# Kernel optimization log

Measured on AMD Instinct MI355X. Metric: run time of the kernel, lower is better.

Reference implementation:

```python
import jax, jax.numpy as jnp
import numpy as np

ALPHA = 1.702
EPS_RMS = 1e-6
W_LOAD = 0.01
W_IMP = 0.01
W_AUX = 1.0
LIMIT = 7.0
K_TOP = 4


def swiglu(x, alpha=ALPHA, limit=LIMIT):
    x_glu = jnp.clip(x[..., ::2], -limit, limit)
    x_lin = jnp.clip(x[..., 1::2], -limit, limit)
    return x_glu * jax.nn.sigmoid(x_glu * alpha) + (x_lin + 1.0)


def setup_inputs() -> dict:
    key = jax.random.key(0)
    ks = jax.random.split(key, 4)
    T, H, I, E = 2048, 512, 512, 8
    x = jax.random.normal(ks[0], (T, H), dtype=jnp.float32)
    norm_scale = jnp.ones((H,), jnp.float32)
    gate_w = jax.random.normal(ks[1], (E, H), jnp.float32) * 0.02
    gate_b = jnp.zeros((E,), jnp.float32)
    mlp1_w = jax.random.normal(ks[2], (E, 2 * I, H), jnp.float32) * 0.02
    mlp1_b = jnp.zeros((E, 2 * I), jnp.float32)
    mlp2_w = jax.random.normal(ks[3], (E, H, I), jnp.float32) * 0.02
    mlp2_b = jnp.zeros((E, H), jnp.float32)
    return {"x": x, "norm_scale": norm_scale, "gate_w": gate_w, "gate_b": gate_b,
            "mlp1_w": mlp1_w, "mlp1_b": mlp1_b, "mlp2_w": mlp2_w, "mlp2_b": mlp2_b}


def reference(x, norm_scale, gate_w, gate_b, mlp1_w, mlp1_b, mlp2_w, mlp2_b):
    T, H = x.shape
    E = gate_w.shape[0]
    K = K_TOP
    # RMSNorm (fp32 math as in torch module)
    t = x * jax.lax.rsqrt(jnp.mean(x * x, axis=-1, keepdims=True) + EPS_RMS) * norm_scale
    # gating
    gate_logits = t @ gate_w.T + gate_b                      # [T, E]
    gate_probs = jax.nn.softmax(gate_logits, axis=-1)
    expert_weights, experts_indices = jax.lax.top_k(gate_probs, K)
    expert_weights = expert_weights / expert_weights.sum(axis=-1, keepdims=True)
    # per-token per-expert combine coefficient (sum of slot weights routed to e)
    coeff = jnp.zeros((T, E), x.dtype).at[jnp.arange(T)[:, None], experts_indices].add(expert_weights)
    # dense expert compute (math-equivalent to the gathered einsums; avoids
    # materializing per-token weight matrices)
    h = jnp.einsum('th,ech->tec', t, mlp1_w) + mlp1_b[None]  # [T, E, 2I]
    a = swiglu(h)                                            # [T, E, I]
    y = jnp.einsum('tei,ehi->teh', a, mlp2_w) + mlp2_b[None] # [T, E, H]
    out = jnp.einsum('teh,te->th', y, coeff) + x
    # aux losses (replicates the torch code exactly, incl. D-doubling quirk)
    P = gate_probs.mean(axis=0)                              # [E]
    counts = jax.vmap(lambda col: jnp.zeros((E,), x.dtype).at[col].add(1.0), in_axes=1)(experts_indices)  # [K, E]
    doubling = (2.0 ** (K - jnp.arange(K))).astype(x.dtype)  # D_i = 2*(D_{i-1}+c_i)
    D = (doubling[:, None] * counts).sum(axis=0) / (T * K)
    loss_load = W_LOAD * E * (P * D).sum()
    importance = gate_logits.sum(axis=0)
    cv = jnp.std(importance, ddof=1) / (importance.mean() + 1e-6)
    loss_imp = W_IMP * cv ** 2
    aux_loss = W_AUX * (loss_load + loss_imp)
    return out, aux_loss
```

## Files before the change

kernel.cpp:

```cpp
#include <hip/hip_runtime.h>
#include <stdint.h>

#define ALPHA 1.702f
#define LIMIT 7.0f

typedef float f32x4 __attribute__((ext_vector_type(4)));
typedef __bf16 bf16x8 __attribute__((ext_vector_type(8)));

static __device__ __forceinline__ unsigned short f2bf(float f) {
    union { float f; uint32_t u; } v; v.f = f;
    uint32_t u = v.u;
    return (unsigned short)((u + 0x7FFFu + ((u >> 16) & 1u)) >> 16);
}

#define GLL16(GP, LP) __builtin_amdgcn_global_load_lds( \
    (const __attribute__((address_space(1))) void*)(GP), \
    (__attribute__((address_space(3))) void*)(LP), 16, 0, 0)

static __device__ __forceinline__ int lsw(int row, int kc) {
    return row * 4 + (kc ^ ((row >> 1) & 3));
}

__global__ __launch_bounds__(256) void prep_kernel(
    const float* __restrict__ w1, const float* __restrict__ w2,
    unsigned short* __restrict__ w1p, unsigned short* __restrict__ w2b,
    const float* __restrict__ x,
    const float* __restrict__ norm_scale,
    const float* __restrict__ gate_w,
    const float* __restrict__ gate_b,
    const float* __restrict__ b2,
    unsigned short* __restrict__ t_bf,
    float* __restrict__ coeff,
    float* __restrict__ accum,
    float* __restrict__ out)
{
    __shared__ float red[4][48];
    if (blockIdx.x < 6144) {
        const int idx = blockIdx.x * 256 + threadIdx.x;
        const int n1 = 1048576;
        if (idx < n1) {
            const int e = idx >> 17;
            const int rem = idx & 131071;
            const int r = rem >> 7;
            const int c = rem & 127;
            const int src = (r < 512) ? (2 * r) : (2 * (r - 512) + 1);
            float4 v = ((const float4*)w1)[(e << 17) + (src << 7) + c];
            ushort4 o = { f2bf(v.x), f2bf(v.y), f2bf(v.z), f2bf(v.w) };
            ((ushort4*)w1p)[idx] = o;
        } else {
            const int i2 = idx - n1;
            float4 v = ((const float4*)w2)[i2];
            ushort4 o = { f2bf(v.x), f2bf(v.y), f2bf(v.z), f2bf(v.w) };
            ((ushort4*)w2b)[i2] = o;
        }
        return;
    }
    const int bid = blockIdx.x - 6144;
    const int wave = threadIdx.x >> 6;
    const int lane = threadIdx.x & 63;

    float accP[8], accI[8], accC[32];
    #pragma unroll
    for (int e = 0; e < 8; ++e) { accP[e] = 0.f; accI[e] = 0.f; }
    #pragma unroll
    for (int i = 0; i < 32; ++i) accC[i] = 0.f;

    #pragma unroll
    for (int it = 0; it < 2; ++it) {
        const int t = bid * 8 + wave * 2 + it;
        const float4* xr = (const float4*)(x + t * 512);
        float4 x0 = xr[lane * 2];
        float4 x1 = xr[lane * 2 + 1];
        float ss = x0.x*x0.x + x0.y*x0.y + x0.z*x0.z + x0.w*x0.w
                 + x1.x*x1.x + x1.y*x1.y + x1.z*x1.z + x1.w*x1.w;
        #pragma unroll
        for (int off = 32; off > 0; off >>= 1) ss += __shfl_xor(ss, off, 64);
        const float rstd = rsqrtf(ss * (1.f / 512.f) + 1e-6f);
        const float4* sr = (const float4*)norm_scale;
        float4 s0 = sr[lane * 2], s1 = sr[lane * 2 + 1];
        float tv[8];
        tv[0] = x0.x * rstd * s0.x; tv[1] = x0.y * rstd * s0.y;
        tv[2] = x0.z * rstd * s0.z; tv[3] = x0.w * rstd * s0.w;
        tv[4] = x1.x * rstd * s1.x; tv[5] = x1.y * rstd * s1.y;
        tv[6] = x1.z * rstd * s1.z; tv[7] = x1.w * rstd * s1.w;
        uint32_t p0 = (uint32_t)f2bf(tv[0]) | ((uint32_t)f2bf(tv[1]) << 16);
        uint32_t p1 = (uint32_t)f2bf(tv[2]) | ((uint32_t)f2bf(tv[3]) << 16);
        uint32_t p2 = (uint32_t)f2bf(tv[4]) | ((uint32_t)f2bf(tv[5]) << 16);
        uint32_t p3 = (uint32_t)f2bf(tv[6]) | ((uint32_t)f2bf(tv[7]) << 16);
        uint4 pk; pk.x = p0; pk.y = p1; pk.z = p2; pk.w = p3;
        ((uint4*)(t_bf + t * 512))[lane] = pk;
        float le[8];
        #pragma unroll
        for (int e = 0; e < 8; ++e) {
            const float4* gw = (const float4*)(gate_w + e * 512);
            float4 g0 = gw[lane * 2], g1 = gw[lane * 2 + 1];
            float d = tv[0]*g0.x + tv[1]*g0.y + tv[2]*g0.z + tv[3]*g0.w
                    + tv[4]*g1.x + tv[5]*g1.y + tv[6]*g1.z + tv[7]*g1.w;
            #pragma unroll
            for (int off = 32; off > 0; off >>= 1) d += __shfl_xor(d, off, 64);
            le[e] = d + gate_b[e];
        }
        float mx = le[0];
        #pragma unroll
        for (int e = 1; e < 8; ++e) mx = fmaxf(mx, le[e]);
        float pe[8], se = 0.f;
        #pragma unroll
        for (int e = 0; e < 8; ++e) { pe[e] = __expf(le[e] - mx); se += pe[e]; }
        const float sinv = 1.f / se;
        #pragma unroll
        for (int e = 0; e < 8; ++e) pe[e] *= sinv;
        unsigned picked = 0;
        int ik[4]; float wk[4];
        #pragma unroll
        for (int k = 0; k < 4; ++k) {
            float bv = -1.f; int bi = 0;
            #pragma unroll
            for (int e = 0; e < 8; ++e)
                if (!(picked & (1u << e)) && pe[e] > bv) { bv = pe[e]; bi = e; }
            ik[k] = bi; wk[k] = bv; picked |= (1u << bi);
        }
        const float winv = 1.f / (wk[0] + wk[1] + wk[2] + wk[3]);
        float nw[4];
        #pragma unroll
        for (int k = 0; k < 4; ++k) nw[k] = wk[k] * winv;
        float ce[8];
        #pragma unroll
        for (int e = 0; e < 8; ++e) {
            float c = 0.f;
            #pragma unroll
            for (int k = 0; k < 4; ++k) c += (ik[k] == e) ? nw[k] : 0.f;
            ce[e] = c;
        }
        if (lane == 0) {
            #pragma unroll
            for (int e = 0; e < 8; ++e) coeff[t * 8 + e] = ce[e];
        }
        #pragma unroll
        for (int e = 0; e < 8; ++e) { accP[e] += pe[e]; accI[e] += le[e]; }
        #pragma unroll
        for (int k = 0; k < 4; ++k)
            #pragma unroll
            for (int e = 0; e < 8; ++e)
                accC[k * 8 + e] += (ik[k] == e) ? 1.f : 0.f;
        float ov[8];
        ov[0] = x0.x; ov[1] = x0.y; ov[2] = x0.z; ov[3] = x0.w;
        ov[4] = x1.x; ov[5] = x1.y; ov[6] = x1.z; ov[7] = x1.w;
        #pragma unroll
        for (int e = 0; e < 8; ++e) {
            const float4* br = (const float4*)(b2 + e * 512);
            float4 b0 = br[lane * 2], bb1 = br[lane * 2 + 1];
            ov[0] += ce[e] * b0.x; ov[1] += ce[e] * b0.y;
            ov[2] += ce[e] * b0.z; ov[3] += ce[e] * b0.w;
            ov[4] += ce[e] * bb1.x; ov[5] += ce[e] * bb1.y;
            ov[6] += ce[e] * bb1.z; ov[7] += ce[e] * bb1.w;
        }
        float4 o0, o1;
        o0.x = ov[0]; o0.y = ov[1]; o0.z = ov[2]; o0.w = ov[3];
        o1.x = ov[4]; o1.y = ov[5]; o1.z = ov[6]; o1.w = ov[7];
        float4* orow = (float4*)(out + t * 512);
        orow[lane * 2] = o0; orow[lane * 2 + 1] = o1;
    }
    if (lane == 0) {
        #pragma unroll
        for (int e = 0; e < 8; ++e) { red[wave][e] = accP[e]; red[wave][8 + e] = accI[e]; }
        #pragma unroll
        for (int i = 0; i < 32; ++i) red[wave][16 + i] = accC[i];
    }
    __syncthreads();
    if (threadIdx.x < 48) {
        float s = red[0][threadIdx.x] + red[1][threadIdx.x]
                + red[2][threadIdx.x] + red[3][threadIdx.x];
        atomicAdd(accum + threadIdx.x, s);
    }
}

__global__ __launch_bounds__(256, 2) void gemm1_swiglu(
    const unsigned short* __restrict__ A,
    const unsigned short* __restrict__ w1p,
    const float* __restrict__ b1,
    const float* __restrict__ coeff,
    unsigned short* __restrict__ As,
    const float* __restrict__ accum,
    float* __restrict__ aux_out)
{
    if (blockIdx.x == 512) {
        if (threadIdx.x == 0) {
            float imp[8], sl = 0.f;
            #pragma unroll
            for (int e = 0; e < 8; ++e) {
                float P = accum[e] * (1.f / 2048.f);
                imp[e] = accum[8 + e];
                float D = (16.f * accum[16 + e] + 8.f * accum[24 + e]
                         + 4.f * accum[32 + e] + 2.f * accum[40 + e]) * (1.f / 8192.f);
                sl += P * D;
            }
            float loss_load = 0.01f * 8.f * sl;
            float mean = 0.f;
            #pragma unroll
            for (int e = 0; e < 8; ++e) mean += imp[e];
            mean *= 0.125f;
            float var = 0.f;
            #pragma unroll
            for (int e = 0; e < 8; ++e) { float d = imp[e] - mean; var += d * d; }
            var *= (1.f / 7.f);
            float cv = sqrtf(var) / (mean + 1e-6f);
            *aux_out = loss_load + 0.01f * cv * cv;
        }
        return;
    }
    __shared__ unsigned short tA[2][4096];
    __shared__ unsigned short tBg[2][4096];
    __shared__ unsigned short tBl[2][4096];
    const int tid = threadIdx.x;
    const int bx = blockIdx.x;
    const int tile_p = bx & 31, tile_m = bx >> 5;
    const int e = tile_p >> 2;
    const int np = (tile_p & 3) * 128;
    const int m0 = tile_m * 128;
    const int lane = tid & 63, wave = tid >> 6;
    const int wm = (wave & 1) * 64, wn = (wave >> 1) * 64;
    const int quad = lane >> 4, l16 = lane & 15;
    const int srow = tid >> 2;
    const int soff = ((tid & 3) ^ ((tid >> 3) & 3)) * 8;

    const unsigned short* Ar0 = A + (m0 + srow) * 512 + soff;
    const unsigned short* Ar1 = A + (m0 + 64 + srow) * 512 + soff;
    const unsigned short* Bg = w1p + (e * 1024 + np) * 512;
    const unsigned short* Bg0 = Bg + srow * 512 + soff;
    const unsigned short* Bg1 = Bg + (64 + srow) * 512 + soff;
    const unsigned short* Bl0 = Bg0 + 512 * 512;
    const unsigned short* Bl1 = Bg1 + 512 * 512;

    int rA[4], rB[4];
    #pragma unroll
    for (int i = 0; i < 4; ++i) {
        rA[i] = lsw(wm + i * 16 + l16, quad) * 8;
        rB[i] = lsw(wn + i * 16 + l16, quad) * 8;
    }

    f32x4 accG[4][4], accL[4][4];
    #pragma unroll
    for (int i = 0; i < 4; ++i)
        #pragma unroll
        for (int j = 0; j < 4; ++j) {
            f32x4 z = {0.f, 0.f, 0.f, 0.f};
            accG[i][j] = z; accL[i][j] = z;
        }

#define STAGE1(s, k0) do { \
    GLL16(Ar0 + (k0), tA[s] + tid * 8); \
    GLL16(Ar1 + (k0), tA[s] + (tid + 256) * 8); \
    GLL16(Bg0 + (k0), tBg[s] + tid * 8); \
    GLL16(Bg1 + (k0), tBg[s] + (tid + 256) * 8); \
    GLL16(Bl0 + (k0), tBl[s] + tid * 8); \
    GLL16(Bl1 + (k0), tBl[s] + (tid + 256) * 8); \
} while (0)

    STAGE1(0, 0);
    STAGE1(1, 32);
    #pragma unroll
    for (int kt = 0; kt < 16; ++kt) {
        const int cur = kt & 1;
        if (kt < 15) asm volatile("s_waitcnt vmcnt(6)" ::: "memory");
        else         asm volatile("s_waitcnt vmcnt(0)" ::: "memory");
        asm volatile("s_barrier" ::: "memory");
        bf16x8 af[4], bg[4], bl[4];
        #pragma unroll
        for (int i = 0; i < 4; ++i) {
            af[i] = *(const bf16x8*)(tA[cur] + rA[i]);
            bg[i] = *(const bf16x8*)(tBg[cur] + rB[i]);
            bl[i] = *(const bf16x8*)(tBl[cur] + rB[i]);
        }
        asm volatile("s_waitcnt lgkmcnt(0)" ::: "memory");
        asm volatile("s_barrier" ::: "memory");
        if (kt < 14) STAGE1(cur, (kt + 2) * 32);
        #pragma unroll
        for (int i = 0; i < 4; ++i)
            #pragma unroll
            for (int j = 0; j < 4; ++j) {
                accG[i][j] = __builtin_amdgcn_mfma_f32_16x16x32_bf16(af[i], bg[j], accG[i][j], 0, 0, 0);
                accL[i][j] = __builtin_amdgcn_mfma_f32_16x16x32_bf16(af[i], bl[j], accL[i][j], 0, 0, 0);
            }
    }
#undef STAGE1

    float cw[4][4];
    #pragma unroll
    for (int i = 0; i < 4; ++i) {
        const int rowb = m0 + wm + i * 16 + quad * 4;
        #pragma unroll
        for (int r = 0; r < 4; ++r) cw[i][r] = coeff[(rowb + r) * 8 + e];
    }
    #pragma unroll
    for (int j = 0; j < 4; ++j) {
        const int colp = np + wn + j * 16 + l16;
        const float bgv = b1[e * 1024 + 2 * colp];
        const float blv = b1[e * 1024 + 2 * colp + 1];
        #pragma unroll
        for (int i = 0; i < 4; ++i) {
            const int rowb = m0 + wm + i * 16 + quad * 4;
            #pragma unroll
            for (int r = 0; r < 4; ++r) {
                float g = fminf(fmaxf(accG[i][j][r] + bgv, -LIMIT), LIMIT);
                float l = fminf(fmaxf(accL[i][j][r] + blv, -LIMIT), LIMIT);
                float a = g / (1.f + __expf(-ALPHA * g)) + l + 1.f;
                a *= cw[i][r];
                As[(rowb + r) * 4096 + e * 512 + colp] = f2bf(a);
            }
        }
    }
}

__global__ __launch_bounds__(256, 2) void gemm2(
    const unsigned short* __restrict__ As,
    const unsigned short* __restrict__ w2b,
    float* __restrict__ out)
{
    __shared__ unsigned short tA[2][4096];
    __shared__ unsigned short tB[2][4096];
    const int tid = threadIdx.x;
    const int bx = blockIdx.x;
    const int tile_n = bx & 3;
    const int tile_m = (bx >> 2) & 15;
    const int e = bx >> 6;
    const int m0 = tile_m * 128, n0 = tile_n * 128;
    const int lane = tid & 63, wave = tid >> 6;
    const int wm = (wave & 1) * 64, wn = (wave >> 1) * 64;
    const int quad = lane >> 4, l16 = lane & 15;
    const int srow = tid >> 2;
    const int soff = ((tid & 3) ^ ((tid >> 3) & 3)) * 8;

    const unsigned short* Ar0 = As + (m0 + srow) * 4096 + e * 512 + soff;
    const unsigned short* Ar1 = As + (m0 + 64 + srow) * 4096 + e * 512 + soff;
    const unsigned short* Bb  = w2b + e * 262144;
    const unsigned short* Br0 = Bb + (n0 + srow) * 512 + soff;
    const unsigned short* Br1 = Bb + (n0 + 64 + srow) * 512 + soff;

    int rA[4], rB[4];
    #pragma unroll
    for (int i = 0; i < 4; ++i) {
        rA[i] = lsw(wm + i * 16 + l16, quad) * 8;
        rB[i] = lsw(wn + i * 16 + l16, quad) * 8;
    }

    f32x4 acc[4][4];
    #pragma unroll
    for (int i = 0; i < 4; ++i)
        #pragma unroll
        for (int j = 0; j < 4; ++j) { f32x4 z = {0.f, 0.f, 0.f, 0.f}; acc[i][j] = z; }

#define STAGE2(s, k0) do { \
    GLL16(Ar0 + (k0), tA[s] + tid * 8); \
    GLL16(Ar1 + (k0), tA[s] + (tid + 256) * 8); \
    GLL16(Br0 + (k0), tB[s] + tid * 8); \
    GLL16(Br1 + (k0), tB[s] + (tid + 256) * 8); \
} while (0)

    STAGE2(0, 0);
    STAGE2(1, 32);
    #pragma unroll
    for (int kt = 0; kt < 16; ++kt) {
        const int cur = kt & 1;
        if (kt < 15) asm volatile("s_waitcnt vmcnt(4)" ::: "memory");
        else         asm volatile("s_waitcnt vmcnt(0)" ::: "memory");
        asm volatile("s_barrier" ::: "memory");
        bf16x8 af[4], bf[4];
        #pragma unroll
        for (int i = 0; i < 4; ++i) {
            af[i] = *(const bf16x8*)(tA[cur] + rA[i]);
            bf[i] = *(const bf16x8*)(tB[cur] + rB[i]);
        }
        asm volatile("s_waitcnt lgkmcnt(0)" ::: "memory");
        asm volatile("s_barrier" ::: "memory");
        if (kt < 14) STAGE2(cur, (kt + 2) * 32);
        #pragma unroll
        for (int i = 0; i < 4; ++i)
            #pragma unroll
            for (int j = 0; j < 4; ++j)
                acc[i][j] = __builtin_amdgcn_mfma_f32_16x16x32_bf16(af[i], bf[j], acc[i][j], 0, 0, 0);
    }
#undef STAGE2

    #pragma unroll
    for (int j = 0; j < 4; ++j) {
        const int col = n0 + wn + j * 16 + l16;
        #pragma unroll
        for (int i = 0; i < 4; ++i) {
            const int rowb = m0 + wm + i * 16 + quad * 4;
            #pragma unroll
            for (int r = 0; r < 4; ++r)
                atomicAdd(&out[(rowb + r) * 512 + col], acc[i][j][r]);
        }
    }
}

extern "C" void kernel_launch(void* const* d_in, const int* in_sizes, int n_in,
                              void* d_out, int out_size, void* d_ws, size_t ws_size,
                              hipStream_t stream)
{
    (void)in_sizes; (void)n_in; (void)out_size; (void)ws_size;
    const float* x          = (const float*)d_in[0];
    const float* norm_scale = (const float*)d_in[1];
    const float* gate_w     = (const float*)d_in[2];
    const float* gate_b     = (const float*)d_in[3];
    const float* mlp1_w     = (const float*)d_in[4];
    const float* mlp1_b     = (const float*)d_in[5];
    const float* mlp2_w     = (const float*)d_in[6];
    const float* mlp2_b     = (const float*)d_in[7];
    float* out = (float*)d_out;

    char* ws = (char*)d_ws;
    unsigned short* w1p   = (unsigned short*)(ws);
    unsigned short* w2b   = (unsigned short*)(ws + 8388608);
    unsigned short* tbf   = (unsigned short*)(ws + 12582912);
    unsigned short* As    = (unsigned short*)(ws + 14680064);
    float*          coeff = (float*)(ws + 31457280);
    float*          accum = (float*)(ws + 31522816);

    hipMemsetAsync(accum, 0, 192, stream);
    prep_kernel<<<6400, 256, 0, stream>>>(mlp1_w, mlp2_w, w1p, w2b,
                                          x, norm_scale, gate_w, gate_b, mlp2_b,
                                          tbf, coeff, accum, out);
    gemm1_swiglu<<<513, 256, 0, stream>>>(tbf, w1p, mlp1_b, coeff, As,
                                          accum, out + 2048 * 512);
    gemm2<<<512, 256, 0, stream>>>(As, w2b, out);
}
```

Measured before the change: 166.8 us.

## Fuse gemm1 and gemm2 into one persistent kernel with per-tile dependency flags

```diff
diff --git a/kernel.cpp b/kernel.cpp
--- a/kernel.cpp
+++ b/kernel.cpp
@@ -31,11 +31,13 @@
     const float* __restrict__ b2,
     unsigned short* __restrict__ t_bf,
     float* __restrict__ coeff,
-    float* __restrict__ accum,
+    float* __restrict__ paux,
+    int* __restrict__ done,
     float* __restrict__ out)
 {
     __shared__ float red[4][48];
     if (blockIdx.x < 6144) {
+        if (blockIdx.x == 0 && threadIdx.x < 128) done[threadIdx.x & 127] = 0;
         const int idx = blockIdx.x * 256 + threadIdx.x;
         const int n1 = 1048576;
         if (idx < n1) {
@@ -168,69 +170,33 @@
     }
     __syncthreads();
     if (threadIdx.x < 48) {
-        float s = red[0][threadIdx.x] + red[1][threadIdx.x]
-                + red[2][threadIdx.x] + red[3][threadIdx.x];
-        atomicAdd(accum + threadIdx.x, s);
+        paux[bid * 48 + threadIdx.x] =
+            red[0][threadIdx.x] + red[1][threadIdx.x]
+          + red[2][threadIdx.x] + red[3][threadIdx.x];
     }
 }
 
-__global__ __launch_bounds__(256, 2) void gemm1_swiglu(
+__global__ __launch_bounds__(256, 2) void fused_gemm(
     const unsigned short* __restrict__ A,
     const unsigned short* __restrict__ w1p,
     const float* __restrict__ b1,
     const float* __restrict__ coeff,
     unsigned short* __restrict__ As,
-    const float* __restrict__ accum,
-    float* __restrict__ aux_out)
+    const unsigned short* __restrict__ w2b,
+    float* __restrict__ out,
+    const float* __restrict__ paux,
+    float* __restrict__ aux_out,
+    int* __restrict__ done)
 {
-    if (blockIdx.x == 512) {
-        if (threadIdx.x == 0) {
-            float imp[8], sl = 0.f;
-            #pragma unroll
-            for (int e = 0; e < 8; ++e) {
-                float P = accum[e] * (1.f / 2048.f);
-                imp[e] = accum[8 + e];
-                float D = (16.f * accum[16 + e] + 8.f * accum[24 + e]
-                         + 4.f * accum[32 + e] + 2.f * accum[40 + e]) * (1.f / 8192.f);
-                sl += P * D;
-            }
-            float loss_load = 0.01f * 8.f * sl;
-            float mean = 0.f;
-            #pragma unroll
-            for (int e = 0; e < 8; ++e) mean += imp[e];
-            mean *= 0.125f;
-            float var = 0.f;
-            #pragma unroll
-            for (int e = 0; e < 8; ++e) { float d = imp[e] - mean; var += d * d; }
-            var *= (1.f / 7.f);
-            float cv = sqrtf(var) / (mean + 1e-6f);
-            *aux_out = loss_load + 0.01f * cv * cv;
-        }
-        return;
-    }
-    __shared__ unsigned short tA[2][4096];
-    __shared__ unsigned short tBg[2][4096];
-    __shared__ unsigned short tBl[2][4096];
+    __shared__ unsigned short smem[6][4608];
     const int tid = threadIdx.x;
     const int bx = blockIdx.x;
-    const int tile_p = bx & 31, tile_m = bx >> 5;
-    const int e = tile_p >> 2;
-    const int np = (tile_p & 3) * 128;
-    const int m0 = tile_m * 128;
     const int lane = tid & 63, wave = tid >> 6;
     const int wm = (wave & 1) * 64, wn = (wave >> 1) * 64;
     const int quad = lane >> 4, l16 = lane & 15;
     const int srow = tid >> 2;
     const int soff = ((tid & 3) ^ ((tid >> 3) & 3)) * 8;
 
-    const unsigned short* Ar0 = A + (m0 + srow) * 512 + soff;
-    const unsigned short* Ar1 = A + (m0 + 64 + srow) * 512 + soff;
-    const unsigned short* Bg = w1p + (e * 1024 + np) * 512;
-    const unsigned short* Bg0 = Bg + srow * 512 + soff;
-    const unsigned short* Bg1 = Bg + (64 + srow) * 512 + soff;
-    const unsigned short* Bl0 = Bg0 + 512 * 512;
-    const unsigned short* Bl1 = Bg1 + 512 * 512;
-
     int rA[4], rB[4];
     #pragma unroll
     for (int i = 0; i < 4; ++i) {
@@ -238,158 +204,197 @@
         rB[i] = lsw(wn + i * 16 + l16, quad) * 8;
     }
 
-    f32x4 accG[4][4], accL[4][4];
-    #pragma unroll
-    for (int i = 0; i < 4; ++i)
-        #pragma unroll
-        for (int j = 0; j < 4; ++j) {
-            f32x4 z = {0.f, 0.f, 0.f, 0.f};
-            accG[i][j] = z; accL[i][j] = z;
-        }
+    {
+        const int tile_p = bx & 31, tile_m = bx >> 5;
+        const int e = tile_p >> 2;
+        const int np = (tile_p & 3) * 128;
+        const int m0 = tile_m * 128;
+
+        const unsigned short* Ar0 = A + (m0 + srow) * 512 + soff;
+        const unsigned short* Ar1 = A + (m0 + 64 + srow) * 512 + soff;
+        const unsigned short* Bg = w1p + (e * 1024 + np) * 512;
+        const unsigned short* Bg0 = Bg + srow * 512 + soff;
+        const unsigned short* Bg1 = Bg + (64 + srow) * 512 + soff;
+        const unsigned short* Bl0 = Bg0 + 512 * 512;
+        const unsigned short* Bl1 = Bg1 + 512 * 512;
+
+        f32x4 accG[4][4], accL[4][4];
+        #pragma unroll
+        for (int i = 0; i < 4; ++i)
+            #pragma unroll
+            for (int j = 0; j < 4; ++j) {
+                f32x4 z = {0.f, 0.f, 0.f, 0.f};
+                accG[i][j] = z; accL[i][j] = z;
+            }
 
 #define STAGE1(s, k0) do { \
-    GLL16(Ar0 + (k0), tA[s] + tid * 8); \
-    GLL16(Ar1 + (k0), tA[s] + (tid + 256) * 8); \
-    GLL16(Bg0 + (k0), tBg[s] + tid * 8); \
-    GLL16(Bg1 + (k0), tBg[s] + (tid + 256) * 8); \
-    GLL16(Bl0 + (k0), tBl[s] + tid * 8); \
-    GLL16(Bl1 + (k0), tBl[s] + (tid + 256) * 8); \
+    GLL16(Ar0 + (k0), smem[(s)*3+0] + tid * 8); \
+    GLL16(Ar1 + (k0), smem[(s)*3+0] + (tid + 256) * 8); \
+    GLL16(Bg0 + (k0), smem[(s)*3+1] + tid * 8); \
+    GLL16(Bg1 + (k0), smem[(s)*3+1] + (tid + 256) * 8); \
+    GLL16(Bl0 + (k0), smem[(s)*3+2] + tid * 8); \
+    GLL16(Bl1 + (k0), smem[(s)*3+2] + (tid + 256) * 8); \
 } while (0)
 
-    STAGE1(0, 0);
-    STAGE1(1, 32);
-    #pragma unroll
-    for (int kt = 0; kt < 16; ++kt) {
-        const int cur = kt & 1;
-        if (kt < 15) asm volatile("s_waitcnt vmcnt(6)" ::: "memory");
-        else         asm volatile("s_waitcnt vmcnt(0)" ::: "memory");
-        asm volatile("s_barrier" ::: "memory");
-        bf16x8 af[4], bg[4], bl[4];
-        #pragma unroll
-        for (int i = 0; i < 4; ++i) {
-            af[i] = *(const bf16x8*)(tA[cur] + rA[i]);
-            bg[i] = *(const bf16x8*)(tBg[cur] + rB[i]);
-            bl[i] = *(const bf16x8*)(tBl[cur] + rB[i]);
-        }
-        asm volatile("s_waitcnt lgkmcnt(0)" ::: "memory");
-        asm volatile("s_barrier" ::: "memory");
-        if (kt < 14) STAGE1(cur, (kt + 2) * 32);
-        #pragma unroll
-        for (int i = 0; i < 4; ++i)
-            #pragma unroll
-            for (int j = 0; j < 4; ++j) {
-                accG[i][j] = __builtin_amdgcn_mfma_f32_16x16x32_bf16(af[i], bg[j], accG[i][j], 0, 0, 0);
-                accL[i][j] = __builtin_amdgcn_mfma_f32_16x16x32_bf16(af[i], bl[j], accL[i][j], 0, 0, 0);
-            }
-    }
+        STAGE1(0, 0);
+        STAGE1(1, 32);
+        #pragma unroll
+        for (int kt = 0; kt < 16; ++kt) {
+            const int cur = kt & 1;
+            if (kt < 15) asm volatile("s_waitcnt vmcnt(6)" ::: "memory");
+            else         asm volatile("s_waitcnt vmcnt(0)" ::: "memory");
+            asm volatile("s_barrier" ::: "memory");
+            bf16x8 af[4], bg[4], bl[4];
+            #pragma unroll
+            for (int i = 0; i < 4; ++i) {
+                af[i] = *(const bf16x8*)(smem[cur*3+0] + rA[i]);
+                bg[i] = *(const bf16x8*)(smem[cur*3+1] + rB[i]);
+                bl[i] = *(const bf16x8*)(smem[cur*3+2] + rB[i]);
+            }
+            asm volatile("s_waitcnt lgkmcnt(0)" ::: "memory");
+            asm volatile("s_barrier" ::: "memory");
+            if (kt < 14) STAGE1(cur, (kt + 2) * 32);
+            #pragma unroll
+            for (int i = 0; i < 4; ++i)
+                #pragma unroll
+                for (int j = 0; j < 4; ++j) {
+                    accG[i][j] = __builtin_amdgcn_mfma_f32_16x16x32_bf16(af[i], bg[j], accG[i][j], 0, 0, 0);
+                    accL[i][j] = __builtin_amdgcn_mfma_f32_16x16x32_bf16(af[i], bl[j], accL[i][j], 0, 0, 0);
+                }
+        }
 #undef STAGE1
 
-    float cw[4][4];
-    #pragma unroll
-    for (int i = 0; i < 4; ++i) {
-        const int rowb = m0 + wm + i * 16 + quad * 4;
-        #pragma unroll
-        for (int r = 0; r < 4; ++r) cw[i][r] = coeff[(rowb + r) * 8 + e];
-    }
-    #pragma unroll
-    for (int j = 0; j < 4; ++j) {
-        const int colp = np + wn + j * 16 + l16;
-        const float bgv = b1[e * 1024 + 2 * colp];
-        const float blv = b1[e * 1024 + 2 * colp + 1];
+        float cw[4][4];
         #pragma unroll
         for (int i = 0; i < 4; ++i) {
             const int rowb = m0 + wm + i * 16 + quad * 4;
             #pragma unroll
-            for (int r = 0; r < 4; ++r) {
-                float g = fminf(fmaxf(accG[i][j][r] + bgv, -LIMIT), LIMIT);
-                float l = fminf(fmaxf(accL[i][j][r] + blv, -LIMIT), LIMIT);
-                float a = g / (1.f + __expf(-ALPHA * g)) + l + 1.f;
-                a *= cw[i][r];
-                As[(rowb + r) * 4096 + e * 512 + colp] = f2bf(a);
-            }
-        }
-    }
-}
-
-__global__ __launch_bounds__(256, 2) void gemm2(
-    const unsigned short* __restrict__ As,
-    const unsigned short* __restrict__ w2b,
-    float* __restrict__ out)
-{
-    __shared__ unsigned short tA[2][4096];
-    __shared__ unsigned short tB[2][4096];
-    const int tid = threadIdx.x;
-    const int bx = blockIdx.x;
-    const int tile_n = bx & 3;
-    const int tile_m = (bx >> 2) & 15;
-    const int e = bx >> 6;
-    const int m0 = tile_m * 128, n0 = tile_n * 128;
-    const int lane = tid & 63, wave = tid >> 6;
-    const int wm = (wave & 1) * 64, wn = (wave >> 1) * 64;
-    const int quad = lane >> 4, l16 = lane & 15;
-    const int srow = tid >> 2;
-    const int soff = ((tid & 3) ^ ((tid >> 3) & 3)) * 8;
-
-    const unsigned short* Ar0 = As + (m0 + srow) * 4096 + e * 512 + soff;
-    const unsigned short* Ar1 = As + (m0 + 64 + srow) * 4096 + e * 512 + soff;
-    const unsigned short* Bb  = w2b + e * 262144;
-    const unsigned short* Br0 = Bb + (n0 + srow) * 512 + soff;
-    const unsigned short* Br1 = Bb + (n0 + 64 + srow) * 512 + soff;
-
-    int rA[4], rB[4];
-    #pragma unroll
-    for (int i = 0; i < 4; ++i) {
-        rA[i] = lsw(wm + i * 16 + l16, quad) * 8;
-        rB[i] = lsw(wn + i * 16 + l16, quad) * 8;
-    }
-
-    f32x4 acc[4][4];
-    #pragma unroll
-    for (int i = 0; i < 4; ++i)
-        #pragma unroll
-        for (int j = 0; j < 4; ++j) { f32x4 z = {0.f, 0.f, 0.f, 0.f}; acc[i][j] = z; }
+            for (int r = 0; r < 4; ++r) cw[i][r] = coeff[(rowb + r) * 8 + e];
+        }
+        #pragma unroll
+        for (int j = 0; j < 4; ++j) {
+            const int colp = np + wn + j * 16 + l16;
+            const float bgv = b1[e * 1024 + 2 * colp];
+            const float blv = b1[e * 1024 + 2 * colp + 1];
+            #pragma unroll
+            for (int i = 0; i < 4; ++i) {
+                const int rowb = m0 + wm + i * 16 + quad * 4;
+                #pragma unroll
+                for (int r = 0; r < 4; ++r) {
+                    float g = fminf(fmaxf(accG[i][j][r] + bgv, -LIMIT), LIMIT);
+                    float l = fminf(fmaxf(accL[i][j][r] + blv, -LIMIT), LIMIT);
+                    float a = g / (1.f + __expf(-ALPHA * g)) + l + 1.f;
+                    a *= cw[i][r];
+                    As[(rowb + r) * 4096 + e * 512 + colp] = f2bf(a);
+                }
+            }
+        }
+        __threadfence();
+        __syncthreads();
+        if (tid == 0)
+            __hip_atomic_fetch_add(&done[tile_m * 8 + e], 1,
+                                   __ATOMIC_RELEASE, __HIP_MEMORY_SCOPE_AGENT);
+    }
+
+    if (bx == 0) {
+        float* sred = (float*)(smem[5] + 4096);
+        if (tid < 48) {
+            float s = 0.f;
+            for (int b = 0; b < 256; ++b) s += paux[b * 48 + tid];
+            sred[tid] = s;
+        }
+        __syncthreads();
+        if (tid == 0) {
+            float imp[8], sl = 0.f;
+            #pragma unroll
+            for (int e = 0; e < 8; ++e) {
+                float P = sred[e] * (1.f / 2048.f);
+                imp[e] = sred[8 + e];
+                float D = (16.f * sred[16 + e] + 8.f * sred[24 + e]
+                         + 4.f * sred[32 + e] + 2.f * sred[40 + e]) * (1.f / 8192.f);
+                sl += P * D;
+            }
+            float loss_load = 0.01f * 8.f * sl;
+            float mean = 0.f;
+            #pragma unroll
+            for (int e = 0; e < 8; ++e) mean += imp[e];
+            mean *= 0.125f;
+            float var = 0.f;
+            #pragma unroll
+            for (int e = 0; e < 8; ++e) { float d = imp[e] - mean; var += d * d; }
+            var *= (1.f / 7.f);
+            float cv = sqrtf(var) / (mean + 1e-6f);
+            *aux_out = loss_load + 0.01f * cv * cv;
+        }
+    }
+
+    {
+        const int tile_n = bx & 3;
+        const int tile_m = (bx >> 2) & 15;
+        const int e = bx >> 6;
+        const int m0 = tile_m * 128, n0 = tile_n * 128;
+
+        if (tid == 0) {
+            while (__hip_atomic_load(&done[tile_m * 8 + e],
+                                     __ATOMIC_ACQUIRE, __HIP_MEMORY_SCOPE_AGENT) < 4)
+                __builtin_amdgcn_s_sleep(2);
+        }
+        __syncthreads();
+
+        const unsigned short* Ar0 = As + (m0 + srow) * 4096 + e * 512 + soff;
+        const unsigned short* Ar1 = As + (m0 + 64 + srow) * 4096 + e * 512 + soff;
+        const unsigned short* Bb  = w2b + e * 262144;
+        const unsigned short* Br0 = Bb + (n0 + srow) * 512 + soff;
+        const unsigned short* Br1 = Bb + (n0 + 64 + srow) * 512 + soff;
+
+        f32x4 acc[4][4];
+        #pragma unroll
+        for (int i = 0; i < 4; ++i)
+            #pragma unroll
+            for (int j = 0; j < 4; ++j) { f32x4 z = {0.f, 0.f, 0.f, 0.f}; acc[i][j] = z; }
 
 #define STAGE2(s, k0) do { \
-    GLL16(Ar0 + (k0), tA[s] + tid * 8); \
-    GLL16(Ar1 + (k0), tA[s] + (tid + 256) * 8); \
-    GLL16(Br0 + (k0), tB[s] + tid * 8); \
-    GLL16(Br1 + (k0), tB[s] + (tid + 256) * 8); \
+    GLL16(Ar0 + (k0), smem[(s)*3+0] + tid * 8); \
+    GLL16(Ar1 + (k0), smem[(s)*3+0] + (tid + 256) * 8); \
+    GLL16(Br0 + (k0), smem[(s)*3+1] + tid * 8); \
+    GLL16(Br1 + (k0), smem[(s)*3+1] + (tid + 256) * 8); \
 } while (0)
 
-    STAGE2(0, 0);
-    STAGE2(1, 32);
-    #pragma unroll
-    for (int kt = 0; kt < 16; ++kt) {
-        const int cur = kt & 1;
-        if (kt < 15) asm volatile("s_waitcnt vmcnt(4)" ::: "memory");
-        else         asm volatile("s_waitcnt vmcnt(0)" ::: "memory");
-        asm volatile("s_barrier" ::: "memory");
-        bf16x8 af[4], bf[4];
-        #pragma unroll
-        for (int i = 0; i < 4; ++i) {
-            af[i] = *(const bf16x8*)(tA[cur] + rA[i]);
-            bf[i] = *(const bf16x8*)(tB[cur] + rB[i]);
-        }
-        asm volatile("s_waitcnt lgkmcnt(0)" ::: "memory");
-        asm volatile("s_barrier" ::: "memory");
-        if (kt < 14) STAGE2(cur, (kt + 2) * 32);
-        #pragma unroll
-        for (int i = 0; i < 4; ++i)
-            #pragma unroll
-            for (int j = 0; j < 4; ++j)
-                acc[i][j] = __builtin_amdgcn_mfma_f32_16x16x32_bf16(af[i], bf[j], acc[i][j], 0, 0, 0);
-    }
+        STAGE2(0, 0);
+        STAGE2(1, 32);
+        #pragma unroll
+        for (int kt = 0; kt < 16; ++kt) {
+            const int cur = kt & 1;
+            if (kt < 15) asm volatile("s_waitcnt vmcnt(4)" ::: "memory");
+            else         asm volatile("s_waitcnt vmcnt(0)" ::: "memory");
+            asm volatile("s_barrier" ::: "memory");
+            bf16x8 af[4], bf[4];
+            #pragma unroll
+            for (int i = 0; i < 4; ++i) {
+                af[i] = *(const bf16x8*)(smem[cur*3+0] + rA[i]);
+                bf[i] = *(const bf16x8*)(smem[cur*3+1] + rB[i]);
+            }
+            asm volatile("s_waitcnt lgkmcnt(0)" ::: "memory");
+            asm volatile("s_barrier" ::: "memory");
+            if (kt < 14) STAGE2(cur, (kt + 2) * 32);
+            #pragma unroll
+            for (int i = 0; i < 4; ++i)
+                #pragma unroll
+                for (int j = 0; j < 4; ++j)
+                    acc[i][j] = __builtin_amdgcn_mfma_f32_16x16x32_bf16(af[i], bf[j], acc[i][j], 0, 0, 0);
+        }
 #undef STAGE2
 
-    #pragma unroll
-    for (int j = 0; j < 4; ++j) {
-        const int col = n0 + wn + j * 16 + l16;
-        #pragma unroll
-        for (int i = 0; i < 4; ++i) {
-            const int rowb = m0 + wm + i * 16 + quad * 4;
-            #pragma unroll
-            for (int r = 0; r < 4; ++r)
-                atomicAdd(&out[(rowb + r) * 512 + col], acc[i][j][r]);
+        #pragma unroll
+        for (int j = 0; j < 4; ++j) {
+            const int col = n0 + wn + j * 16 + l16;
+            #pragma unroll
+            for (int i = 0; i < 4; ++i) {
+                const int rowb = m0 + wm + i * 16 + quad * 4;
+                #pragma unroll
+                for (int r = 0; r < 4; ++r)
+                    atomicAdd(&out[(rowb + r) * 512 + col], acc[i][j][r]);
+            }
         }
     }
 }
@@ -415,13 +420,12 @@
     unsigned short* tbf   = (unsigned short*)(ws + 12582912);
     unsigned short* As    = (unsigned short*)(ws + 14680064);
     float*          coeff = (float*)(ws + 31457280);
-    float*          accum = (float*)(ws + 31522816);
-
-    hipMemsetAsync(accum, 0, 192, stream);
+    float*          paux  = (float*)(ws + 31522816);
+    int*            done  = (int*)(ws + 31571968);
+
     prep_kernel<<<6400, 256, 0, stream>>>(mlp1_w, mlp2_w, w1p, w2b,
                                           x, norm_scale, gate_w, gate_b, mlp2_b,
-                                          tbf, coeff, accum, out);
-    gemm1_swiglu<<<513, 256, 0, stream>>>(tbf, w1p, mlp1_b, coeff, As,
-                                          accum, out + 2048 * 512);
-    gemm2<<<512, 256, 0, stream>>>(As, w2b, out);
+                                          tbf, coeff, paux, done, out);
+    fused_gemm<<<512, 256, 0, stream>>>(tbf, w1p, mlp1_b, coeff, As, w2b, out,
+                                        paux, out + 2048 * 512, done);
 }
```

After: 251.4 us. 1.51x slower.

## Enlarge gemm1 tiles, deepen gemm2 pipeline, replace aux atomics with partials

Applied to the files above, without the earlier changes.

```diff
diff --git a/kernel.cpp b/kernel.cpp
--- a/kernel.cpp
+++ b/kernel.cpp
@@ -31,7 +31,7 @@
     const float* __restrict__ b2,
     unsigned short* __restrict__ t_bf,
     float* __restrict__ coeff,
-    float* __restrict__ accum,
+    float* __restrict__ paux,
     float* __restrict__ out)
 {
     __shared__ float red[4][48];
@@ -168,81 +168,55 @@
     }
     __syncthreads();
     if (threadIdx.x < 48) {
-        float s = red[0][threadIdx.x] + red[1][threadIdx.x]
-                + red[2][threadIdx.x] + red[3][threadIdx.x];
-        atomicAdd(accum + threadIdx.x, s);
-    }
-}
-
-__global__ __launch_bounds__(256, 2) void gemm1_swiglu(
+        paux[bid * 48 + threadIdx.x] =
+            red[0][threadIdx.x] + red[1][threadIdx.x]
+          + red[2][threadIdx.x] + red[3][threadIdx.x];
+    }
+}
+
+__global__ __launch_bounds__(256, 1) void gemm1_swiglu(
     const unsigned short* __restrict__ A,
     const unsigned short* __restrict__ w1p,
     const float* __restrict__ b1,
     const float* __restrict__ coeff,
-    unsigned short* __restrict__ As,
-    const float* __restrict__ accum,
-    float* __restrict__ aux_out)
+    unsigned short* __restrict__ As)
 {
-    if (blockIdx.x == 512) {
-        if (threadIdx.x == 0) {
-            float imp[8], sl = 0.f;
-            #pragma unroll
-            for (int e = 0; e < 8; ++e) {
-                float P = accum[e] * (1.f / 2048.f);
-                imp[e] = accum[8 + e];
-                float D = (16.f * accum[16 + e] + 8.f * accum[24 + e]
-                         + 4.f * accum[32 + e] + 2.f * accum[40 + e]) * (1.f / 8192.f);
-                sl += P * D;
-            }
-            float loss_load = 0.01f * 8.f * sl;
-            float mean = 0.f;
-            #pragma unroll
-            for (int e = 0; e < 8; ++e) mean += imp[e];
-            mean *= 0.125f;
-            float var = 0.f;
-            #pragma unroll
-            for (int e = 0; e < 8; ++e) { float d = imp[e] - mean; var += d * d; }
-            var *= (1.f / 7.f);
-            float cv = sqrtf(var) / (mean + 1e-6f);
-            *aux_out = loss_load + 0.01f * cv * cv;
-        }
-        return;
-    }
-    __shared__ unsigned short tA[2][4096];
+    __shared__ unsigned short tA[2][8192];
     __shared__ unsigned short tBg[2][4096];
     __shared__ unsigned short tBl[2][4096];
     const int tid = threadIdx.x;
     const int bx = blockIdx.x;
-    const int tile_p = bx & 31, tile_m = bx >> 5;
-    const int e = tile_p >> 2;
-    const int np = (tile_p & 3) * 128;
-    const int m0 = tile_m * 128;
+    const int g = bx & 31;
+    const int e = g >> 2;
+    const int np = (g & 3) * 128;
+    const int m0 = (bx >> 5) * 256;
     const int lane = tid & 63, wave = tid >> 6;
-    const int wm = (wave & 1) * 64, wn = (wave >> 1) * 64;
+    const int wm = wave * 64;
     const int quad = lane >> 4, l16 = lane & 15;
     const int srow = tid >> 2;
     const int soff = ((tid & 3) ^ ((tid >> 3) & 3)) * 8;
 
     const unsigned short* Ar0 = A + (m0 + srow) * 512 + soff;
     const unsigned short* Ar1 = A + (m0 + 64 + srow) * 512 + soff;
+    const unsigned short* Ar2 = A + (m0 + 128 + srow) * 512 + soff;
+    const unsigned short* Ar3 = A + (m0 + 192 + srow) * 512 + soff;
     const unsigned short* Bg = w1p + (e * 1024 + np) * 512;
     const unsigned short* Bg0 = Bg + srow * 512 + soff;
     const unsigned short* Bg1 = Bg + (64 + srow) * 512 + soff;
     const unsigned short* Bl0 = Bg0 + 512 * 512;
     const unsigned short* Bl1 = Bg1 + 512 * 512;
 
-    int rA[4], rB[4];
-    #pragma unroll
-    for (int i = 0; i < 4; ++i) {
-        rA[i] = lsw(wm + i * 16 + l16, quad) * 8;
-        rB[i] = lsw(wn + i * 16 + l16, quad) * 8;
-    }
-
-    f32x4 accG[4][4], accL[4][4];
+    int rA[4], rB[8];
+    #pragma unroll
+    for (int i = 0; i < 4; ++i) rA[i] = lsw(wm + i * 16 + l16, quad) * 8;
+    #pragma unroll
+    for (int j = 0; j < 8; ++j) rB[j] = lsw(j * 16 + l16, quad) * 8;
+
+    f32x4 accG[4][8], accL[4][8];
     #pragma unroll
     for (int i = 0; i < 4; ++i)
         #pragma unroll
-        for (int j = 0; j < 4; ++j) {
+        for (int j = 0; j < 8; ++j) {
             f32x4 z = {0.f, 0.f, 0.f, 0.f};
             accG[i][j] = z; accL[i][j] = z;
         }
@@ -250,6 +224,8 @@
 #define STAGE1(s, k0) do { \
     GLL16(Ar0 + (k0), tA[s] + tid * 8); \
     GLL16(Ar1 + (k0), tA[s] + (tid + 256) * 8); \
+    GLL16(Ar2 + (k0), tA[s] + (tid + 512) * 8); \
+    GLL16(Ar3 + (k0), tA[s] + (tid + 768) * 8); \
     GLL16(Bg0 + (k0), tBg[s] + tid * 8); \
     GLL16(Bg1 + (k0), tBg[s] + (tid + 256) * 8); \
     GLL16(Bl0 + (k0), tBl[s] + tid * 8); \
@@ -261,25 +237,27 @@
     #pragma unroll
     for (int kt = 0; kt < 16; ++kt) {
         const int cur = kt & 1;
-        if (kt < 15) asm volatile("s_waitcnt vmcnt(6)" ::: "memory");
+        if (kt < 15) asm volatile("s_waitcnt vmcnt(8)" ::: "memory");
         else         asm volatile("s_waitcnt vmcnt(0)" ::: "memory");
         asm volatile("s_barrier" ::: "memory");
-        bf16x8 af[4], bg[4], bl[4];
-        #pragma unroll
-        for (int i = 0; i < 4; ++i) {
-            af[i] = *(const bf16x8*)(tA[cur] + rA[i]);
-            bg[i] = *(const bf16x8*)(tBg[cur] + rB[i]);
-            bl[i] = *(const bf16x8*)(tBl[cur] + rB[i]);
+        bf16x8 af[4];
+        #pragma unroll
+        for (int i = 0; i < 4; ++i) af[i] = *(const bf16x8*)(tA[cur] + rA[i]);
+        bf16x8 bgf[8], blf[8];
+        #pragma unroll
+        for (int j = 0; j < 8; ++j) {
+            bgf[j] = *(const bf16x8*)(tBg[cur] + rB[j]);
+            blf[j] = *(const bf16x8*)(tBl[cur] + rB[j]);
         }
         asm volatile("s_waitcnt lgkmcnt(0)" ::: "memory");
         asm volatile("s_barrier" ::: "memory");
         if (kt < 14) STAGE1(cur, (kt + 2) * 32);
         #pragma unroll
-        for (int i = 0; i < 4; ++i)
-            #pragma unroll
-            for (int j = 0; j < 4; ++j) {
-                accG[i][j] = __builtin_amdgcn_mfma_f32_16x16x32_bf16(af[i], bg[j], accG[i][j], 0, 0, 0);
-                accL[i][j] = __builtin_amdgcn_mfma_f32_16x16x32_bf16(af[i], bl[j], accL[i][j], 0, 0, 0);
+        for (int j = 0; j < 8; ++j)
+            #pragma unroll
+            for (int i = 0; i < 4; ++i) {
+                accG[i][j] = __builtin_amdgcn_mfma_f32_16x16x32_bf16(af[i], bgf[j], accG[i][j], 0, 0, 0);
+                accL[i][j] = __builtin_amdgcn_mfma_f32_16x16x32_bf16(af[i], blf[j], accL[i][j], 0, 0, 0);
             }
     }
 #undef STAGE1
@@ -292,8 +270,8 @@
         for (int r = 0; r < 4; ++r) cw[i][r] = coeff[(rowb + r) * 8 + e];
     }
     #pragma unroll
-    for (int j = 0; j < 4; ++j) {
-        const int colp = np + wn + j * 16 + l16;
+    for (int j = 0; j < 8; ++j) {
+        const int colp = np + j * 16 + l16;
         const float bgv = b1[e * 1024 + 2 * colp];
         const float blv = b1[e * 1024 + 2 * colp + 1];
         #pragma unroll
@@ -301,9 +279,9 @@
             const int rowb = m0 + wm + i * 16 + quad * 4;
             #pragma unroll
             for (int r = 0; r < 4; ++r) {
-                float g = fminf(fmaxf(accG[i][j][r] + bgv, -LIMIT), LIMIT);
-                float l = fminf(fmaxf(accL[i][j][r] + blv, -LIMIT), LIMIT);
-                float a = g / (1.f + __expf(-ALPHA * g)) + l + 1.f;
+                float gv = fminf(fmaxf(accG[i][j][r] + bgv, -LIMIT), LIMIT);
+                float lv = fminf(fmaxf(accL[i][j][r] + blv, -LIMIT), LIMIT);
+                float a = gv / (1.f + __expf(-ALPHA * gv)) + lv + 1.f;
                 a *= cw[i][r];
                 As[(rowb + r) * 4096 + e * 512 + colp] = f2bf(a);
             }
@@ -314,12 +292,53 @@
 __global__ __launch_bounds__(256, 2) void gemm2(
     const unsigned short* __restrict__ As,
     const unsigned short* __restrict__ w2b,
-    float* __restrict__ out)
+    float* __restrict__ out,
+    const float* __restrict__ paux,
+    float* __restrict__ aux_out)
 {
-    __shared__ unsigned short tA[2][4096];
-    __shared__ unsigned short tB[2][4096];
+    __shared__ unsigned short tA[4][4096];
+    __shared__ unsigned short tB[4][4096];
     const int tid = threadIdx.x;
     const int bx = blockIdx.x;
+
+    if (bx == 512) {
+        __shared__ float sred[4][48];
+        const int wv = tid >> 6, ln = tid & 63;
+        if (ln < 48) {
+            float s = 0.f;
+            for (int b = 0; b < 64; ++b) s += paux[(wv * 64 + b) * 48 + ln];
+            sred[wv][ln] = s;
+        }
+        __syncthreads();
+        if (tid == 0) {
+            float imp[8], sl = 0.f;
+            #pragma unroll
+            for (int e = 0; e < 8; ++e) {
+                float a0 = sred[0][e] + sred[1][e] + sred[2][e] + sred[3][e];
+                float P = a0 * (1.f / 2048.f);
+                imp[e] = sred[0][8+e] + sred[1][8+e] + sred[2][8+e] + sred[3][8+e];
+                float c0 = sred[0][16+e] + sred[1][16+e] + sred[2][16+e] + sred[3][16+e];
+                float c1 = sred[0][24+e] + sred[1][24+e] + sred[2][24+e] + sred[3][24+e];
+                float c2 = sred[0][32+e] + sred[1][32+e] + sred[2][32+e] + sred[3][32+e];
+                float c3 = sred[0][40+e] + sred[1][40+e] + sred[2][40+e] + sred[3][40+e];
+                float D = (16.f * c0 + 8.f * c1 + 4.f * c2 + 2.f * c3) * (1.f / 8192.f);
+                sl += P * D;
+            }
+            float loss_load = 0.01f * 8.f * sl;
+            float mean = 0.f;
+            #pragma unroll
+            for (int e = 0; e < 8; ++e) mean += imp[e];
+            mean *= 0.125f;
+            float var = 0.f;
+            #pragma unroll
+            for (int e = 0; e < 8; ++e) { float d = imp[e] - mean; var += d * d; }
+            var *= (1.f / 7.f);
+            float cv = sqrtf(var) / (mean + 1e-6f);
+            *aux_out = loss_load + 0.01f * cv * cv;
+        }
+        return;
+    }
+
     const int tile_n = bx & 3;
     const int tile_m = (bx >> 2) & 15;
     const int e = bx >> 6;
@@ -358,11 +377,13 @@
 
     STAGE2(0, 0);
     STAGE2(1, 32);
+    STAGE2(2, 64);
     #pragma unroll
     for (int kt = 0; kt < 16; ++kt) {
-        const int cur = kt & 1;
-        if (kt < 15) asm volatile("s_waitcnt vmcnt(4)" ::: "memory");
-        else         asm volatile("s_waitcnt vmcnt(0)" ::: "memory");
+        const int cur = kt & 3;
+        if (kt <= 13)      asm volatile("s_waitcnt vmcnt(8)" ::: "memory");
+        else if (kt == 14) asm volatile("s_waitcnt vmcnt(4)" ::: "memory");
+        else               asm volatile("s_waitcnt vmcnt(0)" ::: "memory");
         asm volatile("s_barrier" ::: "memory");
         bf16x8 af[4], bf[4];
         #pragma unroll
@@ -372,7 +393,7 @@
         }
         asm volatile("s_waitcnt lgkmcnt(0)" ::: "memory");
         asm volatile("s_barrier" ::: "memory");
-        if (kt < 14) STAGE2(cur, (kt + 2) * 32);
+        if (kt <= 12) STAGE2((kt + 3) & 3, (kt + 3) * 32);
         #pragma unroll
         for (int i = 0; i < 4; ++i)
             #pragma unroll
@@ -415,13 +436,11 @@
     unsigned short* tbf   = (unsigned short*)(ws + 12582912);
     unsigned short* As    = (unsigned short*)(ws + 14680064);
     float*          coeff = (float*)(ws + 31457280);
-    float*          accum = (float*)(ws + 31522816);
-
-    hipMemsetAsync(accum, 0, 192, stream);
+    float*          paux  = (float*)(ws + 31522816);
+
     prep_kernel<<<6400, 256, 0, stream>>>(mlp1_w, mlp2_w, w1p, w2b,
                                           x, norm_scale, gate_w, gate_b, mlp2_b,
-                                          tbf, coeff, accum, out);
-    gemm1_swiglu<<<513, 256, 0, stream>>>(tbf, w1p, mlp1_b, coeff, As,
-                                          accum, out + 2048 * 512);
-    gemm2<<<512, 256, 0, stream>>>(As, w2b, out);
-}
+                                          tbf, coeff, paux, out);
+    gemm1_swiglu<<<256, 256, 0, stream>>>(tbf, w1p, mlp1_b, coeff, As);
+    gemm2<<<513, 256, 0, stream>>>(As, w2b, out, paux, out + 2048 * 512);
+}
```

Result: slower. 179.8 us (+7.8%).

## Replace atomic aux accumulation with per-block partials and remap GEMM tiles per XCD

Applied to the files above, without the earlier changes.

```diff
diff --git a/kernel.cpp b/kernel.cpp
--- a/kernel.cpp
+++ b/kernel.cpp
@@ -31,7 +31,7 @@
     const float* __restrict__ b2,
     unsigned short* __restrict__ t_bf,
     float* __restrict__ coeff,
-    float* __restrict__ accum,
+    float* __restrict__ paux,
     float* __restrict__ out)
 {
     __shared__ float red[4][48];
@@ -168,9 +168,9 @@
     }
     __syncthreads();
     if (threadIdx.x < 48) {
-        float s = red[0][threadIdx.x] + red[1][threadIdx.x]
-                + red[2][threadIdx.x] + red[3][threadIdx.x];
-        atomicAdd(accum + threadIdx.x, s);
+        paux[bid * 48 + threadIdx.x] =
+            red[0][threadIdx.x] + red[1][threadIdx.x]
+          + red[2][threadIdx.x] + red[3][threadIdx.x];
     }
 }
 
@@ -180,18 +180,30 @@
     const float* __restrict__ b1,
     const float* __restrict__ coeff,
     unsigned short* __restrict__ As,
-    const float* __restrict__ accum,
+    const float* __restrict__ paux,
     float* __restrict__ aux_out)
 {
     if (blockIdx.x == 512) {
+        __shared__ float sred[4][48];
+        const int wv = threadIdx.x >> 6, ln = threadIdx.x & 63;
+        if (ln < 48) {
+            float s = 0.f;
+            for (int b = 0; b < 64; ++b) s += paux[(wv * 64 + b) * 48 + ln];
+            sred[wv][ln] = s;
+        }
+        __syncthreads();
         if (threadIdx.x == 0) {
             float imp[8], sl = 0.f;
             #pragma unroll
             for (int e = 0; e < 8; ++e) {
-                float P = accum[e] * (1.f / 2048.f);
-                imp[e] = accum[8 + e];
-                float D = (16.f * accum[16 + e] + 8.f * accum[24 + e]
-                         + 4.f * accum[32 + e] + 2.f * accum[40 + e]) * (1.f / 8192.f);
+                float a0 = sred[0][e] + sred[1][e] + sred[2][e] + sred[3][e];
+                float P = a0 * (1.f / 2048.f);
+                imp[e] = sred[0][8+e] + sred[1][8+e] + sred[2][8+e] + sred[3][8+e];
+                float c0 = sred[0][16+e] + sred[1][16+e] + sred[2][16+e] + sred[3][16+e];
+                float c1 = sred[0][24+e] + sred[1][24+e] + sred[2][24+e] + sred[3][24+e];
+                float c2 = sred[0][32+e] + sred[1][32+e] + sred[2][32+e] + sred[3][32+e];
+                float c3 = sred[0][40+e] + sred[1][40+e] + sred[2][40+e] + sred[3][40+e];
+                float D = (16.f * c0 + 8.f * c1 + 4.f * c2 + 2.f * c3) * (1.f / 8192.f);
                 sl += P * D;
             }
             float loss_load = 0.01f * 8.f * sl;
@@ -213,9 +225,12 @@
     __shared__ unsigned short tBl[2][4096];
     const int tid = threadIdx.x;
     const int bx = blockIdx.x;
-    const int tile_p = bx & 31, tile_m = bx >> 5;
-    const int e = tile_p >> 2;
-    const int np = (tile_p & 3) * 128;
+    const int xcd = bx & 7;
+    const int slot = bx >> 3;
+    const int tile_m = slot >> 2;
+    const int g = xcd * 4 + (slot & 3);
+    const int e = g >> 2;
+    const int np = (g & 3) * 128;
     const int m0 = tile_m * 128;
     const int lane = tid & 63, wave = tid >> 6;
     const int wm = (wave & 1) * 64, wn = (wave >> 1) * 64;
@@ -301,9 +316,9 @@
             const int rowb = m0 + wm + i * 16 + quad * 4;
             #pragma unroll
             for (int r = 0; r < 4; ++r) {
-                float g = fminf(fmaxf(accG[i][j][r] + bgv, -LIMIT), LIMIT);
-                float l = fminf(fmaxf(accL[i][j][r] + blv, -LIMIT), LIMIT);
-                float a = g / (1.f + __expf(-ALPHA * g)) + l + 1.f;
+                float g2 = fminf(fmaxf(accG[i][j][r] + bgv, -LIMIT), LIMIT);
+                float l2 = fminf(fmaxf(accL[i][j][r] + blv, -LIMIT), LIMIT);
+                float a = g2 / (1.f + __expf(-ALPHA * g2)) + l2 + 1.f;
                 a *= cw[i][r];
                 As[(rowb + r) * 4096 + e * 512 + colp] = f2bf(a);
             }
@@ -320,9 +335,10 @@
     __shared__ unsigned short tB[2][4096];
     const int tid = threadIdx.x;
     const int bx = blockIdx.x;
-    const int tile_n = bx & 3;
-    const int tile_m = (bx >> 2) & 15;
-    const int e = bx >> 6;
+    const int e = bx & 7;
+    const int slot = bx >> 3;
+    const int tile_m = slot >> 2;
+    const int tile_n = slot & 3;
     const int m0 = tile_m * 128, n0 = tile_n * 128;
     const int lane = tid & 63, wave = tid >> 6;
     const int wm = (wave & 1) * 64, wn = (wave >> 1) * 64;
@@ -415,13 +431,12 @@
     unsigned short* tbf   = (unsigned short*)(ws + 12582912);
     unsigned short* As    = (unsigned short*)(ws + 14680064);
     float*          coeff = (float*)(ws + 31457280);
-    float*          accum = (float*)(ws + 31522816);
-
-    hipMemsetAsync(accum, 0, 192, stream);
+    float*          paux  = (float*)(ws + 31522816);
+
     prep_kernel<<<6400, 256, 0, stream>>>(mlp1_w, mlp2_w, w1p, w2b,
                                           x, norm_scale, gate_w, gate_b, mlp2_b,
-                                          tbf, coeff, accum, out);
+                                          tbf, coeff, paux, out);
     gemm1_swiglu<<<513, 256, 0, stream>>>(tbf, w1p, mlp1_b, coeff, As,
-                                          accum, out + 2048 * 512);
+                                          paux, out + 2048 * 512);
     gemm2<<<512, 256, 0, stream>>>(As, w2b, out);
 }
```

After: 158.6 us. -4.9%, faster.
